# Optimization experiments

Hardware: AMD Instinct MI355X
Metric: run time of the kernel (lower is better)

## Reference

```python
import jax, jax.numpy as jnp
import numpy as np

B, S, HS = 2, 2048, 2048
H, KVH, D = 8, 1, 256
ROPE_BASE = 10000.0


def _rope_cos_sin(position_ids, dim, base=ROPE_BASE):
    # position_ids: (B, S) int -> cos/sin: (B, S, dim)
    inv_freq = 1.0 / (base ** (jnp.arange(0, dim, 2, dtype=jnp.float32) / dim))
    thetas = position_ids.astype(jnp.float32)[..., None] * inv_freq  # (B,S,dim/2)
    emb = jnp.concatenate([thetas, thetas], axis=-1)  # (B,S,dim)
    return jnp.cos(emb), jnp.sin(emb)


def _rotate_half(x):
    x1, x2 = jnp.split(x, 2, axis=-1)
    return jnp.concatenate([-x2, x1], axis=-1)


def _apply_rope(q, k, cos, sin):
    # q,k: (B,h,S,D); cos,sin: (B,S,D) -> unsqueeze head dim
    cos = cos[:, None, :, :]
    sin = sin[:, None, :, :]
    q_emb = q * cos + _rotate_half(q) * sin
    k_emb = k * cos + _rotate_half(k) * sin
    return q_emb, k_emb


def setup_inputs() -> dict:
    key = jax.random.key(0)
    k0, k1, k2, k3, k4 = jax.random.split(key, 5)
    hidden_states = jax.random.normal(k0, (B, S, HS), jnp.float32)
    # causal additive mask: 0 where j<=i, large negative otherwise
    causal = jnp.tril(jnp.ones((S, S), dtype=bool))
    attention_mask = jnp.where(causal, 0.0, -1e9).astype(jnp.float32)
    attention_mask = jnp.broadcast_to(attention_mask[None, None], (B, 1, S, S))
    position_ids = jnp.broadcast_to(jnp.arange(S, dtype=jnp.int32)[None], (B, S))
    scale = 0.02
    Wq = jax.random.normal(k1, (HS, H * D), jnp.float32) * scale
    Wk = jax.random.normal(k2, (HS, KVH * D), jnp.float32) * scale
    Wv = jax.random.normal(k3, (HS, KVH * D), jnp.float32) * scale
    Wo = jax.random.normal(k4, (H * D, HS), jnp.float32) * scale
    return {"hidden_states": hidden_states, "attention_mask": attention_mask,
            "position_ids": position_ids, "Wq": Wq, "Wk": Wk, "Wv": Wv, "Wo": Wo}


def reference(hidden_states, attention_mask, position_ids, Wq, Wk, Wv, Wo):
    bs, seq_len, _ = hidden_states.shape
    q = (hidden_states @ Wq).reshape(bs, seq_len, H, D).transpose(0, 2, 1, 3)     # (B,H,S,D)
    k = (hidden_states @ Wk).reshape(bs, seq_len, KVH, D).transpose(0, 2, 1, 3)   # (B,KVH,S,D)
    v = (hidden_states @ Wv).reshape(bs, seq_len, KVH, D).transpose(0, 2, 1, 3)
    cos, sin = _rope_cos_sin(position_ids, D)
    q, k = _apply_rope(q, k, cos, sin)
    n_rep = H // KVH
    k = jnp.repeat(k, n_rep, axis=1)  # GQA repeat -> (B,H,S,D)
    v = jnp.repeat(v, n_rep, axis=1)
    scores = jnp.einsum('bhqd,bhkd->bhqk', q, k) / jnp.sqrt(jnp.float32(D))
    scores = scores + attention_mask
    attn = jax.nn.softmax(scores.astype(jnp.float32), axis=-1).astype(q.dtype)
    out = jnp.einsum('bhqk,bhkd->bhqd', attn, v)            # (B,H,S,D)
    out = out.transpose(0, 2, 1, 3).reshape(bs, seq_len, H * D)
    return out @ Wo
```

## Files before the change

kernel.cpp:

```cpp
#include <hip/hip_runtime.h>
#include <hip/hip_bf16.h>

typedef __bf16 bf16x8 __attribute__((ext_vector_type(8)));
typedef __bf16 bf16x4 __attribute__((ext_vector_type(4)));
typedef float  f32x4  __attribute__((ext_vector_type(4)));

#define MFMA16(a, b, c) __builtin_amdgcn_mfma_f32_16x16x32_bf16((a), (b), (c), 0, 0, 0)

#define GLOBAL_AS(p) ((const __attribute__((address_space(1))) void*)(p))
#define LDS_AS(p)    ((__attribute__((address_space(3))) void*)(p))

__global__ __launch_bounds__(256) void cvt_bf16_kernel(const float* __restrict__ in,
                                                       __bf16* __restrict__ out)
{
    const int idx = blockIdx.x * 256 + threadIdx.x;
    const float4* p = (const float4*)in + (size_t)idx * 2;
    float4 a = p[0], b = p[1];
    bf16x8 o;
    o[0] = (__bf16)a.x; o[1] = (__bf16)a.y; o[2] = (__bf16)a.z; o[3] = (__bf16)a.w;
    o[4] = (__bf16)b.x; o[5] = (__bf16)b.y; o[6] = (__bf16)b.z; o[7] = (__bf16)b.w;
    ((bf16x8*)out)[idx] = o;
}

__global__ __launch_bounds__(128) void trig_kernel(float2* __restrict__ cs)
{
    const int s = blockIdx.x, i = threadIdx.x;
    const float theta = (float)s * exp2f((float)i * (-13.287712379549449f / 128.f));
    float sn, c;
    sincosf(theta, &sn, &c);
    cs[s * 128 + i] = make_float2(c, sn);
}

__global__ __launch_bounds__(256) void transpose_cvt_kernel(const float* __restrict__ W,
                                                            __bf16* __restrict__ Bt,
                                                            int K, int N)
{
    __shared__ float t[32][33];
    const int n0 = blockIdx.x * 32, k0 = blockIdx.y * 32;
    const int x = threadIdx.x, y = threadIdx.y;
#pragma unroll
    for (int r = 0; r < 4; ++r)
        t[y + r * 8][x] = W[(size_t)(k0 + y + r * 8) * N + n0 + x];
    __syncthreads();
#pragma unroll
    for (int r = 0; r < 4; ++r)
        Bt[(size_t)(n0 + y + r * 8) * K + k0 + x] = (__bf16)t[x][y + r * 8];
}

__global__ __launch_bounds__(256) void vt_kernel(const __bf16* __restrict__ qkv,
                                                 __bf16* __restrict__ vT)
{
    __shared__ __bf16 t[32][33];
    const int s0 = blockIdx.x * 32, d0 = blockIdx.y * 32, b = blockIdx.z;
    const int x = threadIdx.x, y = threadIdx.y;
#pragma unroll
    for (int r = 0; r < 4; ++r)
        t[y + r * 8][x] = qkv[(size_t)(b * 2048 + s0 + y + r * 8) * 2560 + 2304 + d0 + x];
    __syncthreads();
#pragma unroll
    for (int r = 0; r < 4; ++r)
        vT[(size_t)(b * 256 + d0 + y + r * 8) * 2048 + s0 + x] = t[x][y + r * 8];
}

template <typename TC>
__global__ __launch_bounds__(256) void gemm_bt(const __bf16* __restrict__ A,
                                               const __bf16* __restrict__ Bt,
                                               TC* __restrict__ C,
                                               int M, int N, int K)
{
    __shared__ __bf16 As[128 * 32];
    __shared__ __bf16 Bs[128 * 32];

    const int tid  = threadIdx.x;
    const int wave = tid >> 6, lane = tid & 63;
    const int quad = lane >> 4, l16 = lane & 15;
    const int wm = (wave >> 1) * 64, wn = (wave & 1) * 64;
    const int bm = blockIdx.y * 128, bn = blockIdx.x * 128;

    f32x4 acc[4][4] = {};

    for (int k0 = 0; k0 < K; k0 += 32) {
        __syncthreads();
#pragma unroll
        for (int c = 0; c < 2; ++c) {
            const int off = tid * 16 + c * 4096;
            const int row = off >> 6;
            const int kb  = (off & 63) >> 1;
            const __bf16* ga = A  + (size_t)(bm + row) * K + k0 + kb;
            const __bf16* gb = Bt + (size_t)(bn + row) * K + k0 + kb;
            __builtin_amdgcn_global_load_lds(GLOBAL_AS(ga), LDS_AS(As + (off >> 1)), 16, 0, 0);
            __builtin_amdgcn_global_load_lds(GLOBAL_AS(gb), LDS_AS(Bs + (off >> 1)), 16, 0, 0);
        }
        __syncthreads();

        bf16x8 af[4];
#pragma unroll
        for (int mi = 0; mi < 4; ++mi)
            af[mi] = *(const bf16x8*)&As[(wm + mi * 16 + l16) * 32 + quad * 8];
#pragma unroll
        for (int ni = 0; ni < 4; ++ni) {
            bf16x8 bfr = *(const bf16x8*)&Bs[(wn + ni * 16 + l16) * 32 + quad * 8];
#pragma unroll
            for (int mi = 0; mi < 4; ++mi)
                acc[mi][ni] = MFMA16(af[mi], bfr, acc[mi][ni]);
        }
    }
#pragma unroll
    for (int mi = 0; mi < 4; ++mi)
#pragma unroll
        for (int ni = 0; ni < 4; ++ni)
#pragma unroll
            for (int r = 0; r < 4; ++r) {
                int row = bm + wm + mi * 16 + quad * 4 + r;
                int col = bn + wn + ni * 16 + l16;
                C[(size_t)row * N + col] = (TC)acc[mi][ni][r];
            }
}

__global__ __launch_bounds__(256) void rope_kernel(__bf16* __restrict__ qkv,
                                                   const float2* __restrict__ cs)
{
    const int bs = blockIdx.x;
    const int s = bs & 2047;
    const int t = threadIdx.x;
    const float QS = 0.09016843787599907f;

    const int hh = t >> 5, i0 = (t & 31) * 4;
    float2 c0 = cs[s * 128 + i0 + 0], c1 = cs[s * 128 + i0 + 1];
    float2 c2 = cs[s * 128 + i0 + 2], c3 = cs[s * 128 + i0 + 3];

    {
        __bf16* p = qkv + (size_t)bs * 2560 + hh * 256 + i0;
        bf16x4 x1 = *(const bf16x4*)p;
        bf16x4 x2 = *(const bf16x4*)(p + 128);
        bf16x4 o1, o2;
        o1[0] = (__bf16)(((float)x1[0] * c0.x - (float)x2[0] * c0.y) * QS);
        o2[0] = (__bf16)(((float)x2[0] * c0.x + (float)x1[0] * c0.y) * QS);
        o1[1] = (__bf16)(((float)x1[1] * c1.x - (float)x2[1] * c1.y) * QS);
        o2[1] = (__bf16)(((float)x2[1] * c1.x + (float)x1[1] * c1.y) * QS);
        o1[2] = (__bf16)(((float)x1[2] * c2.x - (float)x2[2] * c2.y) * QS);
        o2[2] = (__bf16)(((float)x2[2] * c2.x + (float)x1[2] * c2.y) * QS);
        o1[3] = (__bf16)(((float)x1[3] * c3.x - (float)x2[3] * c3.y) * QS);
        o2[3] = (__bf16)(((float)x2[3] * c3.x + (float)x1[3] * c3.y) * QS);
        *(bf16x4*)p = o1;
        *(bf16x4*)(p + 128) = o2;
    }
    if (t < 32) {
        const int j0 = t * 4;
        float2 d0 = cs[s * 128 + j0 + 0], d1 = cs[s * 128 + j0 + 1];
        float2 d2 = cs[s * 128 + j0 + 2], d3 = cs[s * 128 + j0 + 3];
        __bf16* p = qkv + (size_t)bs * 2560 + 2048 + j0;
        bf16x4 x1 = *(const bf16x4*)p;
        bf16x4 x2 = *(const bf16x4*)(p + 128);
        bf16x4 o1, o2;
        o1[0] = (__bf16)((float)x1[0] * d0.x - (float)x2[0] * d0.y);
        o2[0] = (__bf16)((float)x2[0] * d0.x + (float)x1[0] * d0.y);
        o1[1] = (__bf16)((float)x1[1] * d1.x - (float)x2[1] * d1.y);
        o2[1] = (__bf16)((float)x2[1] * d1.x + (float)x1[1] * d1.y);
        o1[2] = (__bf16)((float)x1[2] * d2.x - (float)x2[2] * d2.y);
        o2[2] = (__bf16)((float)x2[2] * d2.x + (float)x1[2] * d2.y);
        o1[3] = (__bf16)((float)x1[3] * d3.x - (float)x2[3] * d3.y);
        o2[3] = (__bf16)((float)x2[3] * d3.x + (float)x1[3] * d3.y);
        *(bf16x4*)p = o1;
        *(bf16x4*)(p + 128) = o2;
    }
}

__global__ __launch_bounds__(512, 4) void attn_kernel(const __bf16* __restrict__ qkv,
                                                      const __bf16* __restrict__ vTg,
                                                      __bf16* __restrict__ og)
{
    __shared__ __bf16 Ks[64 * 256];
    __shared__ __bf16 Vs[256 * 64];
    __shared__ __bf16 Ps[8][16][36];

    const int b = blockIdx.z, h = blockIdx.y;
    const int xx = (int)blockIdx.x;
    const int half = xx >> 1;
    const bool rev = ((xx & 1) == 0) ^ (b != 0);
    const int qt = rev ? 31 - half : half;
    const int q0 = qt * 64;
    const int tid  = threadIdx.x;
    const int wave = tid >> 6, lane = tid & 63;
    const int quad = lane >> 4, l16 = lane & 15;
    const int xork = l16 & 7;
    const int wq = wave >> 1, wk = wave & 1;

    bf16x8 onef;
#pragma unroll
    for (int e = 0; e < 8; ++e) onef[e] = (__bf16)1.0f;

    const __bf16* qptr = qkv + (size_t)(b * 2048 + q0 + wq * 16 + l16) * 2560 + h * 256;
    bf16x8 qf[8];
#pragma unroll
    for (int dc = 0; dc < 8; ++dc)
        qf[dc] = *(const bf16x8*)(qptr + dc * 32 + quad * 8);

    f32x4 oacc[16] = {};
    f32x4 lacc = {};

    const int kKey0 = tid >> 5;
    const int kC    = (tid & 31) ^ (kKey0 & 7);
    const __bf16* kstage0 = qkv + (size_t)b * 2048 * 2560 + 2048
                          + (size_t)kKey0 * 2560 + kC * 8;
    const int vD0 = tid >> 3;
    const int vC  = (tid & 7) ^ (vD0 & 7);
    const __bf16* vstage0 = vTg + (size_t)b * 256 * 2048 + (size_t)vD0 * 2048 + vC * 8;

    int ckK[8];
#pragma unroll
    for (int dc = 0; dc < 8; ++dc) ckK[dc] = (dc * 4 + quad) ^ xork;
    const int chV = (wk * 4 + quad) ^ xork;

    for (int j0 = 0; j0 <= q0; j0 += 64) {
        __syncthreads();
        const __bf16* kst = kstage0 + (size_t)j0 * 2560;
        const __bf16* vst = vstage0 + j0;
#pragma unroll
        for (int p = 0; p < 4; ++p)
            __builtin_amdgcn_global_load_lds(GLOBAL_AS(kst + (size_t)p * 16 * 2560),
                                             LDS_AS(Ks + tid * 8 + p * 4096), 16, 0, 0);
#pragma unroll
        for (int p = 0; p < 4; ++p)
            __builtin_amdgcn_global_load_lds(GLOBAL_AS(vst + (size_t)p * 64 * 2048),
                                             LDS_AS(Vs + tid * 8 + p * 4096), 16, 0, 0);
        __syncthreads();

        f32x4 sc[2] = {};
        __builtin_amdgcn_s_setprio(1);
#pragma unroll
        for (int nt = 0; nt < 2; ++nt) {
            const __bf16* krow = &Ks[(wk * 32 + nt * 16 + l16) * 256];
#pragma unroll
            for (int dc = 0; dc < 8; ++dc) {
                bf16x8 kf = *(const bf16x8*)(krow + ckK[dc] * 8);
                sc[nt] = MFMA16(qf[dc], kf, sc[nt]);
            }
        }
        __builtin_amdgcn_s_setprio(0);
        if (j0 == q0) {
#pragma unroll
            for (int nt = 0; nt < 2; ++nt) {
                int key = j0 + wk * 32 + nt * 16 + l16;
#pragma unroll
                for (int r = 0; r < 4; ++r) {
                    int row = q0 + wq * 16 + quad * 4 + r;
                    if (key > row) sc[nt][r] = -1e30f;
                }
            }
        }
#pragma unroll
        for (int nt = 0; nt < 2; ++nt)
#pragma unroll
            for (int r = 0; r < 4; ++r)
                Ps[wave][quad * 4 + r][nt * 16 + l16] = (__bf16)exp2f(sc[nt][r] - 8.f);
        bf16x8 pf = *(const bf16x8*)&Ps[wave][l16][quad * 8];
        __builtin_amdgcn_s_setprio(1);
#pragma unroll
        for (int dt = 0; dt < 16; ++dt) {
            const __bf16* vrow = &Vs[(dt * 16 + l16) * 64];
            bf16x8 vf = *(const bf16x8*)(vrow + chV * 8);
            oacc[dt] = MFMA16(pf, vf, oacc[dt]);
        }
        lacc = MFMA16(pf, onef, lacc);
        __builtin_amdgcn_s_setprio(0);
    }

    __syncthreads();
    float* oscr = (wq < 2) ? ((float*)Ks + wq * 4096)
                           : ((float*)Vs + (wq - 2) * 4096);
    float* lscr = (float*)Ps;
    if (wk == 1) {
#pragma unroll
        for (int dt = 0; dt < 16; ++dt)
#pragma unroll
            for (int r = 0; r < 4; ++r)
                oscr[(quad * 4 + r) * 256 + dt * 16 + l16] = oacc[dt][r];
#pragma unroll
        for (int r = 0; r < 4; ++r)
            lscr[(wq * 16 + quad * 4 + r) * 16 + l16] = lacc[r];
    }
    __syncthreads();
    if (wk == 0) {
        float invl[4];
#pragma unroll
        for (int r = 0; r < 4; ++r)
            invl[r] = 1.f / (lacc[r] + lscr[(wq * 16 + quad * 4 + r) * 16 + l16]);
#pragma unroll
        for (int dt = 0; dt < 16; ++dt)
#pragma unroll
            for (int r = 0; r < 4; ++r) {
                float o = oacc[dt][r] + oscr[(quad * 4 + r) * 256 + dt * 16 + l16];
                int row = q0 + wq * 16 + quad * 4 + r;
                int col = h * 256 + dt * 16 + l16;
                og[(size_t)(b * 2048 + row) * 2048 + col] = (__bf16)(o * invl[r]);
            }
    }
}

extern "C" void kernel_launch(void* const* d_in, const int* in_sizes, int n_in,
                              void* d_out, int out_size, void* d_ws, size_t ws_size,
                              hipStream_t stream)
{
    (void)in_sizes; (void)n_in; (void)out_size; (void)ws_size;
    const float* hidden = (const float*)d_in[0];
    const float* Wq = (const float*)d_in[3];
    const float* Wk = (const float*)d_in[4];
    const float* Wv = (const float*)d_in[5];
    const float* Wo = (const float*)d_in[6];

    char* ws = (char*)d_ws;
    __bf16* hb    = (__bf16*)(ws);
    __bf16* qkv   = (__bf16*)(ws + (16u << 20));
    __bf16* vTb   = (__bf16*)(ws + (36u << 20));
    __bf16* ob    = (__bf16*)(ws + (38u << 20));
    __bf16* Wqkvt = (__bf16*)(ws + (54u << 20));
    __bf16* Wot   = (__bf16*)(ws + (64u << 20));
    float2* csb   = (float2*)(ws + (72u << 20));
    float* out = (float*)d_out;

    dim3 blk(256);
    dim3 tblk(32, 8);
    cvt_bf16_kernel<<<dim3(4096), blk, 0, stream>>>(hidden, hb);
    trig_kernel<<<dim3(2048), dim3(128), 0, stream>>>(csb);
    transpose_cvt_kernel<<<dim3(64, 64), tblk, 0, stream>>>(Wq, Wqkvt, 2048, 2048);
    transpose_cvt_kernel<<<dim3(8, 64), tblk, 0, stream>>>(Wk, Wqkvt + (size_t)2048 * 2048, 2048, 256);
    transpose_cvt_kernel<<<dim3(8, 64), tblk, 0, stream>>>(Wv, Wqkvt + (size_t)2304 * 2048, 2048, 256);
    transpose_cvt_kernel<<<dim3(64, 64), tblk, 0, stream>>>(Wo, Wot, 2048, 2048);
    gemm_bt<__bf16><<<dim3(20, 32), blk, 0, stream>>>(hb, Wqkvt, qkv, 4096, 2560, 2048);
    rope_kernel<<<dim3(4096), blk, 0, stream>>>(qkv, csb);
    vt_kernel<<<dim3(64, 8, 2), tblk, 0, stream>>>(qkv, vTb);
    attn_kernel<<<dim3(32, 8, 2), dim3(512), 0, stream>>>(qkv, vTb, ob);
    gemm_bt<float><<<dim3(16, 32), blk, 0, stream>>>(ob, Wot, out, 4096, 2048, 2048);
}
```

Measured before the change: 365.1 us.

## Read K/V fragments directly from global memory instead of staging in LDS

The attention kernel no longer stages K and V tiles into shared memory with barriers each iteration. Each wave now loads its MFMA operands straight from global memory (or L2), which removes two block-wide barriers per key tile and cuts LDS use. The final cross-wave reduction is split into two phases so it fits in a smaller float scratch buffer. The cost is redundant global traffic, since the four query-row wave groups each reload the same K/V data, and per-lane loads are more scattered and less coalesced.

```diff
diff --git a/kernel.cpp b/kernel.cpp
--- a/kernel.cpp
+++ b/kernel.cpp
@@ -170,8 +170,7 @@
                                                       const __bf16* __restrict__ vTg,
                                                       __bf16* __restrict__ og)
 {
-    __shared__ __bf16 Ks[64 * 256];
-    __shared__ __bf16 Vs[256 * 64];
+    __shared__ float  Scr[8192];
     __shared__ __bf16 Ps[8][16][36];
 
     const int b = blockIdx.z, h = blockIdx.y;
@@ -183,7 +182,6 @@
     const int tid  = threadIdx.x;
     const int wave = tid >> 6, lane = tid & 63;
     const int quad = lane >> 4, l16 = lane & 15;
-    const int xork = l16 & 7;
     const int wq = wave >> 1, wk = wave & 1;
 
     bf16x8 onef;
@@ -199,41 +197,20 @@
     f32x4 oacc[16] = {};
     f32x4 lacc = {};
 
-    const int kKey0 = tid >> 5;
-    const int kC    = (tid & 31) ^ (kKey0 & 7);
-    const __bf16* kstage0 = qkv + (size_t)b * 2048 * 2560 + 2048
-                          + (size_t)kKey0 * 2560 + kC * 8;
-    const int vD0 = tid >> 3;
-    const int vC  = (tid & 7) ^ (vD0 & 7);
-    const __bf16* vstage0 = vTg + (size_t)b * 256 * 2048 + (size_t)vD0 * 2048 + vC * 8;
-
-    int ckK[8];
-#pragma unroll
-    for (int dc = 0; dc < 8; ++dc) ckK[dc] = (dc * 4 + quad) ^ xork;
-    const int chV = (wk * 4 + quad) ^ xork;
+    const __bf16* kbase = qkv + (size_t)(b * 2048 + wk * 32 + l16) * 2560
+                        + 2048 + quad * 8;
+    const int chV = wk * 4 + quad;
+    const __bf16* vbase = vTg + (size_t)(b * 256 + l16) * 2048 + chV * 8;
 
     for (int j0 = 0; j0 <= q0; j0 += 64) {
-        __syncthreads();
-        const __bf16* kst = kstage0 + (size_t)j0 * 2560;
-        const __bf16* vst = vstage0 + j0;
-#pragma unroll
-        for (int p = 0; p < 4; ++p)
-            __builtin_amdgcn_global_load_lds(GLOBAL_AS(kst + (size_t)p * 16 * 2560),
-                                             LDS_AS(Ks + tid * 8 + p * 4096), 16, 0, 0);
-#pragma unroll
-        for (int p = 0; p < 4; ++p)
-            __builtin_amdgcn_global_load_lds(GLOBAL_AS(vst + (size_t)p * 64 * 2048),
-                                             LDS_AS(Vs + tid * 8 + p * 4096), 16, 0, 0);
-        __syncthreads();
-
         f32x4 sc[2] = {};
         __builtin_amdgcn_s_setprio(1);
 #pragma unroll
         for (int nt = 0; nt < 2; ++nt) {
-            const __bf16* krow = &Ks[(wk * 32 + nt * 16 + l16) * 256];
+            const __bf16* kr = kbase + (size_t)(j0 + nt * 16) * 2560;
 #pragma unroll
             for (int dc = 0; dc < 8; ++dc) {
-                bf16x8 kf = *(const bf16x8*)(krow + ckK[dc] * 8);
+                bf16x8 kf = *(const bf16x8*)(kr + dc * 32);
                 sc[nt] = MFMA16(qf[dc], kf, sc[nt]);
             }
         }
@@ -258,8 +235,7 @@
         __builtin_amdgcn_s_setprio(1);
 #pragma unroll
         for (int dt = 0; dt < 16; ++dt) {
-            const __bf16* vrow = &Vs[(dt * 16 + l16) * 64];
-            bf16x8 vf = *(const bf16x8*)(vrow + chV * 8);
+            bf16x8 vf = *(const bf16x8*)(vbase + (size_t)(dt * 16) * 2048 + j0);
             oacc[dt] = MFMA16(pf, vf, oacc[dt]);
         }
         lacc = MFMA16(pf, onef, lacc);
@@ -267,34 +243,39 @@
     }
 
     __syncthreads();
-    float* oscr = (wq < 2) ? ((float*)Ks + wq * 4096)
-                           : ((float*)Vs + (wq - 2) * 4096);
     float* lscr = (float*)Ps;
+    float* oscr = Scr + (wq & 1) * 4096;
     if (wk == 1) {
-#pragma unroll
-        for (int dt = 0; dt < 16; ++dt)
-#pragma unroll
-            for (int r = 0; r < 4; ++r)
-                oscr[(quad * 4 + r) * 256 + dt * 16 + l16] = oacc[dt][r];
 #pragma unroll
         for (int r = 0; r < 4; ++r)
             lscr[(wq * 16 + quad * 4 + r) * 16 + l16] = lacc[r];
     }
-    __syncthreads();
-    if (wk == 0) {
-        float invl[4];
-#pragma unroll
-        for (int r = 0; r < 4; ++r)
-            invl[r] = 1.f / (lacc[r] + lscr[(wq * 16 + quad * 4 + r) * 16 + l16]);
-#pragma unroll
-        for (int dt = 0; dt < 16; ++dt)
-#pragma unroll
-            for (int r = 0; r < 4; ++r) {
-                float o = oacc[dt][r] + oscr[(quad * 4 + r) * 256 + dt * 16 + l16];
-                int row = q0 + wq * 16 + quad * 4 + r;
-                int col = h * 256 + dt * 16 + l16;
-                og[(size_t)(b * 2048 + row) * 2048 + col] = (__bf16)(o * invl[r]);
-            }
+#pragma unroll
+    for (int p = 0; p < 2; ++p) {
+        if ((wq >> 1) == p && wk == 1) {
+#pragma unroll
+            for (int dt = 0; dt < 16; ++dt)
+#pragma unroll
+                for (int r = 0; r < 4; ++r)
+                    oscr[(quad * 4 + r) * 256 + dt * 16 + l16] = oacc[dt][r];
+        }
+        __syncthreads();
+        if ((wq >> 1) == p && wk == 0) {
+            float invl[4];
+#pragma unroll
+            for (int r = 0; r < 4; ++r)
+                invl[r] = 1.f / (lacc[r] + lscr[(wq * 16 + quad * 4 + r) * 16 + l16]);
+#pragma unroll
+            for (int dt = 0; dt < 16; ++dt)
+#pragma unroll
+                for (int r = 0; r < 4; ++r) {
+                    float o = oacc[dt][r] + oscr[(quad * 4 + r) * 256 + dt * 16 + l16];
+                    int row = q0 + wq * 16 + quad * 4 + r;
+                    int col = h * 256 + dt * 16 + l16;
+                    og[(size_t)(b * 2048 + row) * 2048 + col] = (__bf16)(o * invl[r]);
+                }
+        }
+        __syncthreads();
     }
 }
 
```

After: 586.8 us. 60.7% more time.
